# Kernel optimization log

Measured on AMD Instinct MI355X. Metric: run time of the kernel, lower is better.

The kernel has to match this reference:

```python
import jax, jax.numpy as jnp
import numpy as np
import itertools, string

# Weight space: 2-layer MLP params, flattened in dict-key order (W1, W2, b1, b2).
SPECS = [(0, 1), (1, 2), (1,), (2,)]
N = 1024            # size of each permutable dim (perm ids 0,1,2)
C_IN, C_OUT = 16, 16
NUM_TERMS = [9, 10, 7, 6]   # equivariant basis terms per output leaf


def _set_partitions(elems):
    if not elems:
        yield []
        return
    first, rest = elems[0], elems[1:]
    for part in _set_partitions(rest):
        for i in range(len(part)):
            yield part[:i] + [part[i] + [first]] + part[i + 1:]
        yield part + [[first]]


def gen_basis(out_spec, in_spec, out_dims, x):
    """All permutation-equivariant basis maps from x (*in_dims, c) to (*out_dims, c).
    Basis elements <-> set partitions of (in,out) axis positions sharing a perm id:
    in-axes in a block are diagonalized; in-only blocks are summed; mixed blocks copy
    the axis to the matching out position; out-only blocks broadcast."""
    pos = ([('in', a, p) for a, p in enumerate(in_spec)]
           + [('out', a, p) for a, p in enumerate(out_spec)])
    by_pid = {}
    for q in pos:
        by_pid.setdefault(q[2], []).append(q)
    parts = [list(_set_partitions(by_pid[p])) for p in sorted(by_pid)]
    terms = []
    for combo in itertools.product(*parts):
        blocks = [b for part in combo for b in part]
        pos2b = {(q[0], q[1]): bi for bi, b in enumerate(blocks) for q in b}
        L = string.ascii_lowercase
        in_sub = ''.join(L[pos2b[('in', a)]] for a in range(len(in_spec)))
        mixed = [bi for bi, b in enumerate(blocks)
                 if any(q[0] == 'in' for q in b) and any(q[0] == 'out' for q in b)]
        out_sub = ''.join(L[bi] for bi in mixed)
        # diagonal over repeated in-axes, sum over in-only blocks; z = channel axis
        t = jnp.einsum(f'{in_sub}z->{out_sub}z', x)
        targets = [min(q[1] for q in blocks[bi] if q[0] == 'out') for bi in mixed]
        t = jnp.transpose(t, list(np.argsort(targets)) + [len(mixed)])
        st = sorted(targets)
        for ax in range(len(out_dims)):
            if ax not in st:
                t = jnp.expand_dims(t, ax)
        t = jnp.broadcast_to(t, tuple(out_dims) + (x.shape[-1],))
        for b in blocks:  # diagonal-embed blocks with >1 out axis (not hit for MLP specs)
            outs = sorted(q[1] for q in b if q[0] == 'out')
            for a1, a2 in zip(outs, outs[1:]):
                n = out_dims[a1]
                sh = [1] * (len(out_dims) + 1)
                sh[a1] = n; sh[a2] = n
                t = t * jnp.eye(n, dtype=x.dtype).reshape(sh)
        terms.append(t)
    return terms


def _forward(flat, thetas, biases):
    outs = []
    for i in range(len(flat)):
        out_dims = flat[i].shape[:-1]
        acc = jnp.zeros(tuple(out_dims) + (C_OUT,), dtype=flat[i].dtype)
        k = 0
        for j in range(len(flat)):
            for term in gen_basis(SPECS[i], SPECS[j], out_dims, flat[j]):
                acc = acc + jnp.einsum('...i,io->...o', term, thetas[i][k])
                k += 1
        outs.append(acc + biases[i])
    return tuple(outs)


def setup_inputs() -> dict:
    key = jax.random.key(0)
    ks = jax.random.split(key, 12)
    inp = {
        'W1': jax.random.normal(ks[0], (N, N, C_IN), jnp.float32),
        'W2': jax.random.normal(ks[1], (N, N, C_IN), jnp.float32),
        'b1': jax.random.normal(ks[2], (N, C_IN), jnp.float32),
        'b2': jax.random.normal(ks[3], (N, C_IN), jnp.float32),
    }
    for i, k in enumerate(NUM_TERMS):
        scale = (1.0 / (C_IN * k)) ** 0.5
        inp[f'theta_{i}'] = scale * jax.random.normal(ks[4 + i], (k, C_IN, C_OUT), jnp.float32)
        inp[f'bias_{i}'] = jnp.zeros((C_OUT,), jnp.float32)
    return inp


def reference(W1, W2, b1, b2, theta_0, theta_1, theta_2, theta_3,
              bias_0, bias_1, bias_2, bias_3):
    return _forward([W1, W2, b1, b2],
                    [theta_0, theta_1, theta_2, theta_3],
                    [bias_0, bias_1, bias_2, bias_3])
```

## Files before the change

### kernel.cpp

```cpp
#include <hip/hip_runtime.h>

#define NDIM 1024
#define CH 16
#define ROW_F4 4096

__device__ inline float4 f4add(float4 a, float4 b) {
    return make_float4(a.x + b.x, a.y + b.y, a.z + b.z, a.w + b.w);
}
__device__ inline float4 f4zero() { return make_float4(0.f, 0.f, 0.f, 0.f); }

__global__ __launch_bounds__(256) void k_fused(const float* __restrict__ W1,
                                               const float* __restrict__ W2,
                                               float* __restrict__ rowpart,
                                               float* __restrict__ colpart,
                                               float* __restrict__ tiletot) {
    int t  = threadIdx.x;
    int jt = blockIdx.x, it = blockIdx.y, z = blockIdx.z;
    const float4* base = (const float4*)(z ? W2 : W1)
                       + (size_t)it * 8 * ROW_F4 + jt * 256 + t;
    __shared__ float4 tile[8][258];
    __shared__ float4 rtot[32];
    float4 colacc = f4zero();
#pragma unroll
    for (int r = 0; r < 8; ++r) {
        float4 v = base[(size_t)r * ROW_F4];
        colacc = f4add(colacc, v);
        tile[r][t] = v;
    }
    ((float4*)colpart)[(size_t)(z * 128 + it) * 4096 + jt * 256 + t] = colacc;
    __syncthreads();
    if (t < 32) {
        int r = t >> 2, cq = t & 3;
        float4 s = f4zero();
#pragma unroll
        for (int jl = 0; jl < 64; ++jl) s = f4add(s, tile[r][jl * 4 + cq]);
        ((float4*)rowpart)[(size_t)(z * 16 + jt) * 4096 + (it * 8 + r) * 4 + cq] = s;
        rtot[t] = s;
    }
    __syncthreads();
    if (t < 4) {
        float4 s = f4zero();
#pragma unroll
        for (int r = 0; r < 8; ++r) s = f4add(s, rtot[r * 4 + t]);
        ((float4*)tiletot)[(size_t)(z * 2048 + it * 16 + jt) * 4 + t] = s;
    }
}

__global__ __launch_bounds__(256) void k_reduce(const float* __restrict__ rowpart,
                                                const float* __restrict__ colpart,
                                                const float* __restrict__ tiletot,
                                                const float* __restrict__ b1,
                                                const float* __restrict__ b2,
                                                float* __restrict__ rowsumF,
                                                float* __restrict__ colsumF,
                                                float* __restrict__ sums) {
    int t = threadIdx.x;
    int b = blockIdx.x;
    if (b < 128) {
        const float4* cp = (const float4*)colpart;
        int o = b * 64 + (t & 63);
        int p = t >> 6;
        int z = o >> 12, rem = o & 4095;
        float4 s = f4zero();
#pragma unroll 8
        for (int k = 0; k < 32; ++k)
            s = f4add(s, cp[(size_t)(z * 128 + p * 32 + k) * 4096 + rem]);
        __shared__ float4 lds[256];
        lds[t] = s;
        __syncthreads();
        if (t < 64) {
            float4 r = f4add(f4add(lds[t], lds[t + 64]),
                             f4add(lds[t + 128], lds[t + 192]));
            ((float4*)colsumF)[o] = r;
        }
    } else if (b < 160) {
        const float4* rp = (const float4*)rowpart;
        int o = (b - 128) * 256 + t;
        int z = o >> 12, rem = o & 4095;
        float4 s = f4zero();
#pragma unroll
        for (int k = 0; k < 16; ++k)
            s = f4add(s, rp[(size_t)(z * 16 + k) * 4096 + rem]);
        ((float4*)rowsumF)[o] = s;
    } else if (b == 160) {
        int c = t & 15, p = (t >> 4) & 7, z = t >> 7;
        float s = 0.f;
#pragma unroll 8
        for (int m = 0; m < 256; ++m)
            s += tiletot[(size_t)(z * 2048 + p * 256 + m) * 16 + c];
        __shared__ float ldsA[2][8][16];
        ldsA[z][p][c] = s;
        __syncthreads();
        if (t < 32) {
            int zz = t >> 4, cc = t & 15;
            float r = 0.f;
#pragma unroll
            for (int q = 0; q < 8; ++q) r += ldsA[zz][q][cc];
            sums[zz * 16 + cc] = r;
        }
    } else {
        int w = b - 161;
        const float* src = w ? b2 : b1;
        int c = t & 15, p = t >> 4;
        float s = 0.f;
#pragma unroll 8
        for (int m = 0; m < 64; ++m)
            s += src[(size_t)(p * 64 + m) * 16 + c];
        __shared__ float ldsB[16][16];
        ldsB[p][c] = s;
        __syncthreads();
        if (t < 16) {
            float r = 0.f;
#pragma unroll
            for (int q = 0; q < 16; ++q) r += ldsB[q][t];
            sums[32 + w * 16 + t] = r;
        }
    }
}

__global__ __launch_bounds__(256) void k_smalls(const float* __restrict__ rowsum,
                                                const float* __restrict__ colsum,
                                                const float* __restrict__ sums,
                                                const float* __restrict__ b1,
                                                const float* __restrict__ b2,
                                                const float* __restrict__ th0,
                                                const float* __restrict__ th1,
                                                const float* __restrict__ th2,
                                                const float* __restrict__ th3,
                                                const float* __restrict__ bias0,
                                                const float* __restrict__ bias1,
                                                const float* __restrict__ bias2,
                                                const float* __restrict__ bias3,
                                                float* __restrict__ R0, float* __restrict__ C0,
                                                float* __restrict__ R1, float* __restrict__ C1,
                                                float* __restrict__ out2, float* __restrict__ out3) {
    int gt = blockIdx.x * 256 + threadIdx.x;
    int i = gt >> 4, o = gt & 15;
    const float* rs1 = rowsum + i * 16;
    const float* rs2 = rowsum + 16384 + i * 16;
    const float* cs1 = colsum + i * 16;
    const float* cs2 = colsum + 16384 + i * 16;
    const float* b1i = b1 + i * 16;
    const float* b2i = b2 + i * 16;
    float r0 = 0.f, c0a = 0.f, r1 = 0.f, c1a = 0.f, o2 = 0.f, o3 = 0.f;
    float k0 = 0.f, k1 = 0.f, k2 = 0.f, k3 = 0.f;
#pragma unroll
    for (int c = 0; c < 16; ++c) {
        float sW1 = sums[c], sW2 = sums[16 + c], sb1 = sums[32 + c], sb2 = sums[48 + c];
        r0  += rs1[c] * th0[(1 * 16 + c) * 16 + o];
        c0a += cs1[c] * th0[(2 * 16 + c) * 16 + o]
             + rs2[c] * th0[(4 * 16 + c) * 16 + o]
             + b1i[c] * th0[(6 * 16 + c) * 16 + o];
        k0  += sW1 * th0[(3 * 16 + c) * 16 + o] + sW2 * th0[(5 * 16 + c) * 16 + o]
             + sb1 * th0[(7 * 16 + c) * 16 + o] + sb2 * th0[(8 * 16 + c) * 16 + o];
        r1  += cs1[c] * th1[(0 * 16 + c) * 16 + o]
             + rs2[c] * th1[(3 * 16 + c) * 16 + o]
             + b1i[c] * th1[(6 * 16 + c) * 16 + o];
        c1a += cs2[c] * th1[(4 * 16 + c) * 16 + o]
             + b2i[c] * th1[(8 * 16 + c) * 16 + o];
        k1  += sW1 * th1[(1 * 16 + c) * 16 + o] + sW2 * th1[(5 * 16 + c) * 16 + o]
             + sb1 * th1[(7 * 16 + c) * 16 + o] + sb2 * th1[(9 * 16 + c) * 16 + o];
        o2  += cs1[c] * th2[(0 * 16 + c) * 16 + o]
             + rs2[c] * th2[(2 * 16 + c) * 16 + o]
             + b1i[c] * th2[(4 * 16 + c) * 16 + o];
        k2  += sW1 * th2[(1 * 16 + c) * 16 + o] + sW2 * th2[(3 * 16 + c) * 16 + o]
             + sb1 * th2[(5 * 16 + c) * 16 + o] + sb2 * th2[(6 * 16 + c) * 16 + o];
        o3  += cs2[c] * th3[(1 * 16 + c) * 16 + o]
             + b2i[c] * th3[(4 * 16 + c) * 16 + o];
        k3  += sW1 * th3[(0 * 16 + c) * 16 + o] + sW2 * th3[(2 * 16 + c) * 16 + o]
             + sb1 * th3[(3 * 16 + c) * 16 + o] + sb2 * th3[(5 * 16 + c) * 16 + o];
    }
    R0[gt]   = r0;
    C0[gt]   = c0a + k0 + bias0[o];
    R1[gt]   = r1;
    C1[gt]   = c1a + k1 + bias1[o];
    out2[gt] = o2 + k2 + bias2[o];
    out3[gt] = o3 + k3 + bias3[o];
}

__global__ __launch_bounds__(256) void k_main(const float* __restrict__ W1,
                                              const float* __restrict__ W2,
                                              const float* __restrict__ R0,
                                              const float* __restrict__ C0,
                                              const float* __restrict__ R1,
                                              const float* __restrict__ C1,
                                              const float* __restrict__ th0,
                                              const float* __restrict__ th1,
                                              float* __restrict__ out0,
                                              float* __restrict__ out1) {
    int z = blockIdx.z;
    const float* W  = z ? W2 : W1;
    const float* R  = z ? R1 : R0;
    const float* Cc = z ? C1 : C0;
    const float* TH = z ? th1 : th0;
    float* out      = z ? out1 : out0;

    int t  = threadIdx.x;
    int i  = blockIdx.y;
    int jb = blockIdx.x * 256;

    __shared__ float4 xs[1280];
    __shared__ float  th[256];
    __shared__ float  r[16];
    th[t] = TH[t];
    if (t < 16) r[t] = R[i * 16 + t];

    const float4* Wf4 = (const float4*)W + (size_t)i * 4096 + jb * 4;
    float4*       Of4 = (float4*)out    + (size_t)i * 4096 + jb * 4;

#pragma unroll
    for (int q = 0; q < 4; ++q) {
        int g = t + 256 * q;
        xs[5 * (g >> 2) + (g & 3)] = Wf4[g];
    }
    __syncthreads();

    float x[16];
#pragma unroll
    for (int k = 0; k < 4; ++k) {
        float4 v = xs[5 * t + k];
        x[4 * k] = v.x; x[4 * k + 1] = v.y; x[4 * k + 2] = v.z; x[4 * k + 3] = v.w;
    }
    const float4* cj = (const float4*)(Cc + (jb + t) * 16);
    float4 c0 = cj[0], c1 = cj[1], c2 = cj[2], c3 = cj[3];
    float acc[16] = {c0.x, c0.y, c0.z, c0.w, c1.x, c1.y, c1.z, c1.w,
                     c2.x, c2.y, c2.z, c2.w, c3.x, c3.y, c3.z, c3.w};
#pragma unroll
    for (int o = 0; o < 16; ++o) acc[o] += r[o];
#pragma unroll
    for (int c = 0; c < 16; ++c) {
        float xv = x[c];
#pragma unroll
        for (int o = 0; o < 16; ++o) acc[o] += xv * th[c * 16 + o];
    }
    __syncthreads();
#pragma unroll
    for (int k = 0; k < 4; ++k)
        xs[5 * t + k] = make_float4(acc[4 * k], acc[4 * k + 1],
                                    acc[4 * k + 2], acc[4 * k + 3]);
    __syncthreads();
#pragma unroll
    for (int q = 0; q < 4; ++q) {
        int g = t + 256 * q;
        Of4[g] = xs[5 * (g >> 2) + (g & 3)];
    }
}

extern "C" void kernel_launch(void* const* d_in, const int* in_sizes, int n_in,
                              void* d_out, int out_size, void* d_ws, size_t ws_size,
                              hipStream_t stream) {
    const float* W1    = (const float*)d_in[0];
    const float* W2    = (const float*)d_in[1];
    const float* b1    = (const float*)d_in[2];
    const float* b2    = (const float*)d_in[3];
    const float* th0   = (const float*)d_in[4];
    const float* bias0 = (const float*)d_in[5];
    const float* th1   = (const float*)d_in[6];
    const float* bias1 = (const float*)d_in[7];
    const float* th2   = (const float*)d_in[8];
    const float* bias2 = (const float*)d_in[9];
    const float* th3   = (const float*)d_in[10];
    const float* bias3 = (const float*)d_in[11];

    float* out  = (float*)d_out;
    float* out0 = out;
    float* out1 = out + (size_t)NDIM * NDIM * CH;
    float* out2 = out1 + (size_t)NDIM * NDIM * CH;
    float* out3 = out2 + (size_t)NDIM * CH;

    float* rowpart = out0;
    float* colpart = out0 + 524288;
    float* tiletot = out0 + 4718592;

    float* ws      = (float*)d_ws;
    float* rowsumF = ws;
    float* colsumF = ws + 32768;
    float* sums    = ws + 65536;
    float* R0      = ws + 65600;
    float* C0      = R0 + 16384;
    float* R1      = C0 + 16384;
    float* C1      = R1 + 16384;

    k_fused<<<dim3(16, 128, 2), dim3(256), 0, stream>>>(W1, W2, rowpart, colpart, tiletot);
    k_reduce<<<dim3(163), dim3(256), 0, stream>>>(rowpart, colpart, tiletot, b1, b2,
                                                  rowsumF, colsumF, sums);
    k_smalls<<<dim3(64), dim3(256), 0, stream>>>(rowsumF, colsumF, sums, b1, b2,
                                                 th0, th1, th2, th3,
                                                 bias0, bias1, bias2, bias3,
                                                 R0, C0, R1, C1, out2, out3);
    k_main<<<dim3(4, NDIM, 2), dim3(256), 0, stream>>>(W1, W2, R0, C0, R1, C1,
                                                       th0, th1 + 2 * 256,
                                                       out0, out1);
}
```

Baseline: 89.93 us.

## Process two rows per thread in k_main and drop shared-memory staging

k_main now has each thread load two consecutive j positions (8 float4) straight from global memory into registers, instead of staging W tiles through padded shared memory and writing outputs back through it. Each theta row read from LDS is reused across both positions, and the two staging barriers are removed. The grid is halved in x to match. The cost is higher register pressure and uncoalesced strided float4 accesses (each thread reads 128 contiguous bytes), which may hurt global memory efficiency.

Measured after the change: 120.4 us. 33.9% more time.

```diff
diff --git a/kernel.cpp b/kernel.cpp
--- a/kernel.cpp
+++ b/kernel.cpp
@@ -189,61 +189,62 @@
                                               float* __restrict__ out0,
                                               float* __restrict__ out1) {
     int z = blockIdx.z;
-    const float* W  = z ? W2 : W1;
-    const float* R  = z ? R1 : R0;
-    const float* Cc = z ? C1 : C0;
-    const float* TH = z ? th1 : th0;
-    float* out      = z ? out1 : out0;
+    const float* __restrict__ W  = z ? W2 : W1;
+    const float* __restrict__ R  = z ? R1 : R0;
+    const float* __restrict__ Cc = z ? C1 : C0;
+    const float* __restrict__ TH = z ? th1 : th0;
+    float* __restrict__ out      = z ? out1 : out0;
 
     int t  = threadIdx.x;
     int i  = blockIdx.y;
-    int jb = blockIdx.x * 256;
-
-    __shared__ float4 xs[1280];
-    __shared__ float  th[256];
-    __shared__ float  r[16];
+    int jb = blockIdx.x * 512;
+
+    __shared__ float th[256];
+    __shared__ float r[16];
     th[t] = TH[t];
     if (t < 16) r[t] = R[i * 16 + t];
-
-    const float4* Wf4 = (const float4*)W + (size_t)i * 4096 + jb * 4;
-    float4*       Of4 = (float4*)out    + (size_t)i * 4096 + jb * 4;
-
-#pragma unroll
-    for (int q = 0; q < 4; ++q) {
-        int g = t + 256 * q;
-        xs[5 * (g >> 2) + (g & 3)] = Wf4[g];
-    }
     __syncthreads();
 
-    float x[16];
-#pragma unroll
-    for (int k = 0; k < 4; ++k) {
-        float4 v = xs[5 * t + k];
-        x[4 * k] = v.x; x[4 * k + 1] = v.y; x[4 * k + 2] = v.z; x[4 * k + 3] = v.w;
-    }
-    const float4* cj = (const float4*)(Cc + (jb + t) * 16);
-    float4 c0 = cj[0], c1 = cj[1], c2 = cj[2], c3 = cj[3];
-    float acc[16] = {c0.x, c0.y, c0.z, c0.w, c1.x, c1.y, c1.z, c1.w,
-                     c2.x, c2.y, c2.z, c2.w, c3.x, c3.y, c3.z, c3.w};
-#pragma unroll
-    for (int o = 0; o < 16; ++o) acc[o] += r[o];
+    const float4* Wp = (const float4*)W  + (size_t)i * 4096 + jb * 4 + t * 8;
+    const float4* Cp = (const float4*)Cc + (size_t)jb * 4 + t * 8;
+    float4*       Op = (float4*)out      + (size_t)i * 4096 + jb * 4 + t * 8;
+
+    float4 x[8];
+#pragma unroll
+    for (int k = 0; k < 8; ++k) x[k] = Wp[k];
+
+    float acc[2][16];
+#pragma unroll
+    for (int jj = 0; jj < 2; ++jj) {
+#pragma unroll
+        for (int q = 0; q < 4; ++q) {
+            float4 cv = Cp[jj * 4 + q];
+            acc[jj][q * 4 + 0] = cv.x + r[q * 4 + 0];
+            acc[jj][q * 4 + 1] = cv.y + r[q * 4 + 1];
+            acc[jj][q * 4 + 2] = cv.z + r[q * 4 + 2];
+            acc[jj][q * 4 + 3] = cv.w + r[q * 4 + 3];
+        }
+    }
 #pragma unroll
     for (int c = 0; c < 16; ++c) {
-        float xv = x[c];
-#pragma unroll
-        for (int o = 0; o < 16; ++o) acc[o] += xv * th[c * 16 + o];
-    }
-    __syncthreads();
-#pragma unroll
-    for (int k = 0; k < 4; ++k)
-        xs[5 * t + k] = make_float4(acc[4 * k], acc[4 * k + 1],
-                                    acc[4 * k + 2], acc[4 * k + 3]);
-    __syncthreads();
-#pragma unroll
-    for (int q = 0; q < 4; ++q) {
-        int g = t + 256 * q;
-        Of4[g] = xs[5 * (g >> 2) + (g & 3)];
-    }
+        float tv[16];
+#pragma unroll
+        for (int o = 0; o < 16; ++o) tv[o] = th[c * 16 + o];
+#pragma unroll
+        for (int jj = 0; jj < 2; ++jj) {
+            float4 xd = x[jj * 4 + (c >> 2)];
+            float xv = ((c & 3) == 0) ? xd.x : ((c & 3) == 1) ? xd.y
+                     : ((c & 3) == 2) ? xd.z : xd.w;
+#pragma unroll
+            for (int o = 0; o < 16; ++o) acc[jj][o] += xv * tv[o];
+        }
+    }
+#pragma unroll
+    for (int jj = 0; jj < 2; ++jj)
+#pragma unroll
+        for (int q = 0; q < 4; ++q)
+            Op[jj * 4 + q] = make_float4(acc[jj][q * 4 + 0], acc[jj][q * 4 + 1],
+                                         acc[jj][q * 4 + 2], acc[jj][q * 4 + 3]);
 }
 
 extern "C" void kernel_launch(void* const* d_in, const int* in_sizes, int n_in,
@@ -288,7 +289,7 @@
                                                  th0, th1, th2, th3,
                                                  bias0, bias1, bias2, bias3,
                                                  R0, C0, R1, C1, out2, out3);
-    k_main<<<dim3(4, NDIM, 2), dim3(256), 0, stream>>>(W1, W2, R0, C0, R1, C1,
+    k_main<<<dim3(2, NDIM, 2), dim3(256), 0, stream>>>(W1, W2, R0, C0, R1, C1,
                                                        th0, th1 + 2 * 256,
                                                        out0, out1);
 }
```
